# Kernel optimization log

Hardware: AMD Instinct MI355X
Metric: run time of the kernel (lower is better)

Reference implementation:

```python
import jax, jax.numpy as jnp
import numpy as np

B, S, SE, H, NH = 1, 2048, 2048, 1024, 16
HD = H // NH
INNER = 4 * H
EPS = 1e-5


def layer_norm(x, g, b):
    mu = jnp.mean(x, axis=-1, keepdims=True)
    var = jnp.mean(jnp.square(x - mu), axis=-1, keepdims=True)
    return (x - mu) * jax.lax.rsqrt(var + EPS) * g + b


def split_heads(x):  # [B,T,H] -> [B,NH,T,HD]
    b, t, _ = x.shape
    return x.reshape(b, t, NH, HD).transpose(0, 2, 1, 3)


def merge_heads(x):  # [B,NH,T,HD] -> [B,T,H]
    b, nh, t, hd = x.shape
    return x.transpose(0, 2, 1, 3).reshape(b, t, nh * hd)


def setup_inputs() -> dict:
    key = jax.random.key(0)
    ks = jax.random.split(key, 16)
    n = lambda k, shp: (jax.random.normal(k, shp, jnp.float32) * 0.02)
    return {
        "hidden_states": jax.random.normal(ks[0], (B, S, H), jnp.float32),
        "encoder_hidden_states": jax.random.normal(ks[1], (B, SE, H), jnp.float32),
        "scorer_logits": jax.random.normal(ks[2], (B, SE), jnp.float32),
        "ln1_g": jnp.ones((H,), jnp.float32), "ln1_b": jnp.zeros((H,), jnp.float32),
        "c_attn_w": n(ks[3], (H, 3 * H)), "c_attn_b": jnp.zeros((3 * H,), jnp.float32),
        "attn_proj_w": n(ks[4], (H, H)), "attn_proj_b": jnp.zeros((H,), jnp.float32),
        "lnx_g": jnp.ones((H,), jnp.float32), "lnx_b": jnp.zeros((H,), jnp.float32),
        "q_attn_w": n(ks[5], (H, H)), "q_attn_b": jnp.zeros((H,), jnp.float32),
        "x_kv_w": n(ks[6], (H, 2 * H)), "x_kv_b": jnp.zeros((2 * H,), jnp.float32),
        "x_proj_w": n(ks[7], (H, H)), "x_proj_b": jnp.zeros((H,), jnp.float32),
        "ln2_g": jnp.ones((H,), jnp.float32), "ln2_b": jnp.zeros((H,), jnp.float32),
        "fc_w": n(ks[8], (H, INNER)), "fc_b": jnp.zeros((INNER,), jnp.float32),
        "mlp_proj_w": n(ks[9], (INNER, H)), "mlp_proj_b": jnp.zeros((H,), jnp.float32),
    }


def _attn_core(q, k, v, extra_bias=None, causal_bool=False, tril_diag2_additive=False):
    # q,k,v: [B,NH,T,HD]; eager attention, materializes full score matrix (faithful to source)
    w = jnp.einsum("bhqd,bhkd->bhqk", q, k) / jnp.sqrt(jnp.asarray(HD, q.dtype))
    ql, kl = q.shape[-2], k.shape[-2]
    neg = jnp.finfo(w.dtype).min
    if causal_bool:
        mask = jnp.tril(jnp.ones((ql, kl), bool))  # self-attn boolean causal mask
        w = jnp.where(mask[None, None], w, neg)
    if tril_diag2_additive:
        cm = jnp.tril(jnp.ones((ql, kl), w.dtype), k=2)  # limit_cross_attn: tril diagonal=2
        w = w + jnp.where(cm == 0, neg, jnp.zeros((), w.dtype))[None, None]
    if extra_bias is not None:
        w = w + extra_bias[:, None, None, :]  # scorer_logits additive per-key bias
    w = jax.nn.softmax(w, axis=-1)
    return jnp.einsum("bhqk,bhkd->bhqd", w, v)


def reference(hidden_states, encoder_hidden_states, scorer_logits,
              ln1_g, ln1_b, c_attn_w, c_attn_b, attn_proj_w, attn_proj_b,
              lnx_g, lnx_b, q_attn_w, q_attn_b, x_kv_w, x_kv_b, x_proj_w, x_proj_b,
              ln2_g, ln2_b, fc_w, fc_b, mlp_proj_w, mlp_proj_b):
    # --- self attention ---
    residual = hidden_states
    x = layer_norm(hidden_states, ln1_g, ln1_b)
    qkv = x @ c_attn_w + c_attn_b
    q, k, v = jnp.split(qkv, 3, axis=-1)
    a = _attn_core(split_heads(q), split_heads(k), split_heads(v), causal_bool=True)
    a = merge_heads(a) @ attn_proj_w + attn_proj_b
    hidden_states = a + residual
    # --- cross attention (limit_cross_attn=True, scorer_logits bias) ---
    residual = hidden_states
    x = layer_norm(hidden_states, lnx_g, lnx_b)
    q = x @ q_attn_w + q_attn_b
    kv = encoder_hidden_states @ x_kv_w + x_kv_b
    k, v = jnp.split(kv, 2, axis=-1)
    a = _attn_core(split_heads(q), split_heads(k), split_heads(v),
                   extra_bias=scorer_logits, tril_diag2_additive=True)
    a = merge_heads(a) @ x_proj_w + x_proj_b
    hidden_states = residual + a
    # --- MLP (gelu_new = tanh approx) ---
    residual = hidden_states
    x = layer_norm(hidden_states, ln2_g, ln2_b)
    h = jax.nn.gelu(x @ fc_w + fc_b, approximate=True)
    hidden_states = residual + (h @ mlp_proj_w + mlp_proj_b)
    return hidden_states
```

## Files before the change

kernel.cpp:

```cpp
#include <hip/hip_runtime.h>
#include <stdint.h>

#define H     1024
#define S     2048
#define SEQE  2048
#define NHEAD 16
#define HD    64
#define INNER 4096
#define EPSLN 1e-5f
#define LOG2E 1.44269504089f
#define SCALE2 (0.125f * LOG2E)

typedef __attribute__((ext_vector_type(8))) short short8;
typedef __attribute__((ext_vector_type(4))) float floatx4;

__device__ __forceinline__ float b2f(unsigned short u){
  union { unsigned int i; float f; } v; v.i = ((unsigned int)u) << 16; return v.f;
}
__device__ __forceinline__ unsigned short f2b(float f){
  union { float f; unsigned int i; } v; v.f = f;
  unsigned int x = v.i;
  unsigned int r = (x + 0x7FFFu + ((x >> 16) & 1u)) >> 16;
  return (unsigned short)r;
}
__device__ __forceinline__ float fexp2(float x){ return __builtin_amdgcn_exp2f(x); }
__device__ __forceinline__ float gelu_tanh(float x){
  float x3 = x*x*x;
  float t = tanhf(0.7978845608028654f*(x + 0.044715f*x3));
  return 0.5f*x*(1.0f+t);
}

__device__ __forceinline__ void gld16(const unsigned short* g, unsigned short* l){
  __builtin_amdgcn_global_load_lds(
      (const __attribute__((address_space(1))) unsigned int*)g,
      (__attribute__((address_space(3))) unsigned int*)l,
      16, 0, 0);
}

__global__ __launch_bounds__(256) void k_sniff(
    const unsigned short* __restrict__ p, int* __restrict__ flag){
  __shared__ int any;
  if (threadIdx.x == 0) any = 0;
  __syncthreads();
  int bad = 0;
  for (int i = threadIdx.x; i < 8192; i += 256){
    float v = b2f(p[i]);
    if (!(fabsf(v) < 1e6f)) bad = 1;
  }
  if (bad) any = 1;
  __syncthreads();
  if (threadIdx.x == 0) flag[0] = any;
}

struct PrepT {
  const void* src[7];
  unsigned short* dst[7];
  int R[7], C[7];
  int pre[8];
};
__global__ __launch_bounds__(256) void k_prep_t(PrepT d, const int* __restrict__ flag){
  __shared__ unsigned short t[32][33];
  int b = blockIdx.x;
  int m = 0;
  while (b >= d.pre[m+1]) m++;
  int ti = b - d.pre[m];
  int R = d.R[m], C = d.C[m];
  int tx = threadIdx.x & 31, ty = threadIdx.x >> 5;
  int tilesx = C >> 5;
  int bc = (ti % tilesx) << 5, br = (ti / tilesx) << 5;
  const float* sf = (const float*)d.src[m];
  const unsigned short* sb = (const unsigned short*)d.src[m];
  unsigned short* dst = d.dst[m];
  int fl = flag[0];
  #pragma unroll
  for (int i = 0; i < 4; i++){
    size_t idx = (size_t)(br + ty + i*8) * C + bc + tx;
    t[ty + i*8][tx] = fl ? f2b(sf[idx]) : sb[idx];
  }
  __syncthreads();
  #pragma unroll
  for (int i = 0; i < 4; i++)
    dst[(size_t)(bc + ty + i*8) * R + br + tx] = t[tx][ty + i*8];
}

struct SmallCvt {
  const void* src[16];
  unsigned short* dst[16];
  int n[16];
};
__global__ __launch_bounds__(256) void k_prep_c(
    const void* __restrict__ enc, unsigned short* __restrict__ enc_c,
    const void* __restrict__ hsv, float* __restrict__ hidden,
    SmallCvt sc, const int* __restrict__ flag){
  int b = blockIdx.x, tid = threadIdx.x;
  int fl = flag[0];
  if (b < 8192){
    int i = b*256 + tid;
    enc_c[i] = fl ? f2b(((const float*)enc)[i]) : ((const unsigned short*)enc)[i];
  } else if (b < 16384){
    int i = (b - 8192)*256 + tid;
    hidden[i] = fl ? ((const float*)hsv)[i] : b2f(((const unsigned short*)hsv)[i]);
  } else {
    int t = b - 16384;
    const float* sf = (const float*)sc.src[t];
    const unsigned short* sb = (const unsigned short*)sc.src[t];
    unsigned short* d = sc.dst[t];
    for (int i = tid; i < sc.n[t]; i += 256)
      d[i] = fl ? f2b(sf[i]) : sb[i];
  }
}

__global__ __launch_bounds__(256) void k_layernorm(
    const float* __restrict__ x,
    const unsigned short* __restrict__ g, const unsigned short* __restrict__ bb,
    unsigned short* __restrict__ y){
  __shared__ float scratch[4];
  int row = blockIdx.x, tid = threadIdx.x;
  float v[4];
  #pragma unroll
  for (int i=0;i<4;i++) v[i] = x[(size_t)row*H + tid + i*256];
  float s = v[0]+v[1]+v[2]+v[3];
  for (int o=32;o;o>>=1) s += __shfl_xor(s,o,64);
  int wid = tid>>6, lane = tid&63;
  if (lane==0) scratch[wid]=s;
  __syncthreads();
  float mu = (scratch[0]+scratch[1]+scratch[2]+scratch[3]) * (1.0f/H);
  __syncthreads();
  float q = 0.f;
  #pragma unroll
  for (int i=0;i<4;i++){ float d=v[i]-mu; q += d*d; }
  for (int o=32;o;o>>=1) q += __shfl_xor(q,o,64);
  if (lane==0) scratch[wid]=q;
  __syncthreads();
  float var = (scratch[0]+scratch[1]+scratch[2]+scratch[3]) * (1.0f/H);
  float rstd = rsqrtf(var + EPSLN);
  #pragma unroll
  for (int i=0;i<4;i++){
    int idx = tid + i*256;
    float o = (v[i]-mu)*rstd*b2f(g[idx]) + b2f(bb[idx]);
    y[(size_t)row*H + idx] = f2b(o);
  }
}

__global__ __launch_bounds__(256) void k_gemm64(
    const unsigned short* __restrict__ A, const unsigned short* __restrict__ BT,
    const unsigned short* __restrict__ bias,
    unsigned short* __restrict__ outb, float* __restrict__ resid,
    int M, int N, int K, int mode, const int* __restrict__ flag,
    int vcol0, unsigned short* __restrict__ vtout)
{
  __shared__ __align__(16) unsigned short As[2][64*64];
  __shared__ __align__(16) unsigned short Bs[2][128*64];
  int tid = threadIdx.x;
  int bm0 = blockIdx.y * 64, bn0 = blockIdx.x * 128;
  int wid = tid >> 6, lane = tid & 63;
  int wm = (wid & 1) * 32, wn = (wid >> 1) * 64;
  int fl = (mode == 3) ? flag[0] : 0;
  floatx4 acc[2][4] = {};

  const unsigned short* gp[6];
  int lofs[6];
  int aseg[6];
  int lrow = lane >> 3, lchunk = (lane & 7) ^ lrow;
  #pragma unroll
  for (int t = 0; t < 6; t++){
    int seg = wid * 6 + t;
    if (seg < 8){
      gp[t] = A + (size_t)(bm0 + seg*8 + lrow) * K + lchunk*8;
      lofs[t] = seg * 512;
      aseg[t] = 1;
    } else {
      int s = seg - 8;
      gp[t] = BT + (size_t)(bn0 + s*8 + lrow) * K + lchunk*8;
      lofs[t] = s * 512;
      aseg[t] = 0;
    }
  }

  #pragma unroll
  for (int t = 0; t < 6; t++)
    gld16(gp[t], (aseg[t] ? As[0] : Bs[0]) + lofs[t]);

  int mrow = lane & 15, quad = lane >> 4;
  int ib = 0;
  for (int kt = 0; kt < K; kt += 64, ib ^= 1){
    __syncthreads();
    if (kt + 64 < K){
      #pragma unroll
      for (int t = 0; t < 6; t++)
        gld16(gp[t] + kt + 64, (aseg[t] ? As[ib^1] : Bs[ib^1]) + lofs[t]);
    }
    const unsigned short* Ac = As[ib];
    const unsigned short* Bc = Bs[ib];
    #pragma unroll
    for (int k2 = 0; k2 < 2; k2++){
      short8 af[2], bf[4];
      #pragma unroll
      for (int i = 0; i < 2; i++){
        int r = wm + i*16 + mrow;
        int slot = (k2*4 + quad) ^ (r & 7);
        af[i] = *(const short8*)&Ac[r*64 + slot*8];
      }
      #pragma unroll
      for (int j = 0; j < 4; j++){
        int r = wn + j*16 + mrow;
        int slot = (k2*4 + quad) ^ (r & 7);
        bf[j] = *(const short8*)&Bc[r*64 + slot*8];
      }
      #pragma unroll
      for (int i = 0; i < 2; i++){
        #pragma unroll
        for (int j = 0; j < 4; j++){
          acc[i][j] = __builtin_amdgcn_mfma_f32_16x16x32_bf16(af[i], bf[j], acc[i][j], 0,0,0);
        }
      }
    }
  }

  int colb = mrow, rowb = quad * 4;
  #pragma unroll
  for (int i=0;i<2;i++){
    #pragma unroll
    for (int j=0;j<4;j++){
      int col = bn0 + wn + j*16 + colb;
      float bv = b2f(bias[col]);
      int row0 = bm0 + wm + i*16 + rowb;
      if (mode == 4 && col >= vcol0){
        ushort4 uv;
        uv.x = f2b(acc[i][j][0] + bv);
        uv.y = f2b(acc[i][j][1] + bv);
        uv.z = f2b(acc[i][j][2] + bv);
        uv.w = f2b(acc[i][j][3] + bv);
        *(ushort4*)(vtout + (size_t)(col - vcol0)*M + row0) = uv;
      } else {
        #pragma unroll
        for (int rr=0;rr<4;rr++){
          int row = row0 + rr;
          float v = acc[i][j][rr] + bv;
          size_t off = (size_t)row*N + col;
          if      (mode == 0 || mode == 4){ outb[off] = f2b(v); }
          else if (mode == 1){ outb[off] = f2b(gelu_tanh(v)); }
          else if (mode == 2){ resid[off] += v; }
          else {
            float o = v + resid[off];
            if (fl) ((float*)outb)[off] = o;
            else    outb[off] = f2b(o);
          }
        }
      }
    }
  }
}

__global__ __launch_bounds__(256) void k_gemm64s(
    const unsigned short* __restrict__ A, const unsigned short* __restrict__ BT,
    const unsigned short* __restrict__ bias,
    unsigned short* __restrict__ outb, float* __restrict__ resid,
    int M, int N, int K, int mode, const int* __restrict__ flag)
{
  __shared__ __align__(16) unsigned short As[2][64*64];
  __shared__ __align__(16) unsigned short Bs[2][64*64];
  int tid = threadIdx.x;
  int bm0 = blockIdx.y * 64, bn0 = blockIdx.x * 64;
  int wid = tid >> 6, lane = tid & 63;
  int wm = wid * 16;
  int fl = (mode == 3) ? flag[0] : 0;
  floatx4 acc[4] = {};

  const unsigned short* gp[4];
  int lofs[4];
  int aseg[4];
  int lrow = lane >> 3, lchunk = (lane & 7) ^ lrow;
  #pragma unroll
  for (int t = 0; t < 4; t++){
    int seg = wid * 4 + t;
    if (seg < 8){
      gp[t] = A + (size_t)(bm0 + seg*8 + lrow) * K + lchunk*8;
      lofs[t] = seg * 512;
      aseg[t] = 1;
    } else {
      int s = seg - 8;
      gp[t] = BT + (size_t)(bn0 + s*8 + lrow) * K + lchunk*8;
      lofs[t] = s * 512;
      aseg[t] = 0;
    }
  }

  #pragma unroll
  for (int t = 0; t < 4; t++)
    gld16(gp[t], (aseg[t] ? As[0] : Bs[0]) + lofs[t]);

  int mrow = lane & 15, quad = lane >> 4;
  int ib = 0;
  for (int kt = 0; kt < K; kt += 64, ib ^= 1){
    __syncthreads();
    if (kt + 64 < K){
      #pragma unroll
      for (int t = 0; t < 4; t++)
        gld16(gp[t] + kt + 64, (aseg[t] ? As[ib^1] : Bs[ib^1]) + lofs[t]);
    }
    const unsigned short* Ac = As[ib];
    const unsigned short* Bc = Bs[ib];
    #pragma unroll
    for (int k2 = 0; k2 < 2; k2++){
      short8 af, bf[4];
      {
        int r = wm + mrow;
        int slot = (k2*4 + quad) ^ (r & 7);
        af = *(const short8*)&Ac[r*64 + slot*8];
      }
      #pragma unroll
      for (int j = 0; j < 4; j++){
        int r = j*16 + mrow;
        int slot = (k2*4 + quad) ^ (r & 7);
        bf[j] = *(const short8*)&Bc[r*64 + slot*8];
      }
      #pragma unroll
      for (int j = 0; j < 4; j++)
        acc[j] = __builtin_amdgcn_mfma_f32_16x16x32_bf16(af, bf[j], acc[j], 0,0,0);
    }
  }

  int colb = mrow, rowb = quad * 4;
  #pragma unroll
  for (int j=0;j<4;j++){
    int col = bn0 + j*16 + colb;
    float bv = b2f(bias[col]);
    int row0 = bm0 + wm + rowb;
    #pragma unroll
    for (int rr=0;rr<4;rr++){
      int row = row0 + rr;
      float v = acc[j][rr] + bv;
      size_t off = (size_t)row*N + col;
      if      (mode == 0){ outb[off] = f2b(v); }
      else if (mode == 2){ resid[off] += v; }
      else {
        float o = v + resid[off];
        if (fl) ((float*)outb)[off] = o;
        else    outb[off] = f2b(o);
      }
    }
  }
}

template<int CA, int SCOR>
__global__ __launch_bounds__(256) void k_flash2(
    const unsigned short* __restrict__ qb, int qstride,
    const unsigned short* __restrict__ kb, int kstride,
    const unsigned short* __restrict__ vt,
    const unsigned short* __restrict__ scorer,
    unsigned short* __restrict__ obuf, float* __restrict__ mlbuf, int TOTS)
{
  int t = blockIdx.x, h = blockIdx.y, sp = blockIdx.z;
  int klmax0 = 64*t + 64 + CA; if (klmax0 > S) klmax0 = S;
  int nch = (klmax0 + 63) >> 6;
  int nsp = (nch + 7) >> 3;
  if (sp >= nsp) return;
  int base = 0;
  for (int i = 0; i < t; i++){
    int km = 64*i + 64 + CA; if (km > S) km = S;
    base += (((km + 63) >> 6) + 7) >> 3;
  }
  int pidx = h*TOTS + base + sp;
  int c0 = sp*8, c1 = c0 + 8; if (c1 > nch) c1 = nch;

  __shared__ __align__(16) unsigned short Ks[2][64*64];
  __shared__ __align__(16) unsigned short VTs[2][64*64];
  __shared__ __align__(16) unsigned short Ps[4][16*72];
  __shared__ float scs[2][64];
  int tid = threadIdx.x;
  int q0 = t*64;
  int w = tid >> 6, lane = tid & 63;
  int cn = lane & 15, quad = lane >> 4, kq = quad * 8;
  unsigned short* Pw = Ps[w];
  int srow0 = w*16;
  int lr = lane >> 3;
  int lc = ((lane & 7) ^ lr) * 8;
  const unsigned short* kg0 = kb + (size_t)(srow0 + lr) * kstride + h*HD + lc;
  const unsigned short* kg1 = kb + (size_t)(srow0 + 8 + lr) * kstride + h*HD + lc;
  const unsigned short* vg0 = vt + (size_t)(h*HD + srow0 + lr) * S + lc;
  const unsigned short* vg1 = vt + (size_t)(h*HD + srow0 + 8 + lr) * S + lc;

  const unsigned short* qrow = qb + (size_t)(q0 + w*16 + cn) * qstride + h*HD;
  short8 qf0 = *(const short8*)(qrow + kq);
  short8 qf1 = *(const short8*)(qrow + kq + 32);
  floatx4 oacc[4] = {};
  float l_lane[4] = {0,0,0,0};
  float m_w = -1.0e38f;
  int qmr = q0 + w*16 + quad*4;

  {
    int kc = c0 * 64;
    gld16(kg0 + (size_t)kc * kstride, Ks[0] + srow0*64);
    gld16(kg1 + (size_t)kc * kstride, Ks[0] + (srow0 + 8)*64);
    gld16(vg0 + kc, VTs[0] + srow0*64);
    gld16(vg1 + kc, VTs[0] + (srow0 + 8)*64);
    if (SCOR && tid < 64) scs[0][tid] = b2f(scorer[kc + tid]) * LOG2E;
  }

  int ib = 0;
  for (int ci = c0; ci < c1; ci++, ib ^= 1){
    __syncthreads();
    if (ci + 1 < c1){
      int kn2 = (ci + 1) * 64;
      gld16(kg0 + (size_t)kn2 * kstride, Ks[ib^1] + srow0*64);
      gld16(kg1 + (size_t)kn2 * kstride, Ks[ib^1] + (srow0 + 8)*64);
      gld16(vg0 + kn2, VTs[ib^1] + srow0*64);
      gld16(vg1 + kn2, VTs[ib^1] + (srow0 + 8)*64);
      if (SCOR && tid < 64) scs[ib^1][tid] = b2f(scorer[kn2 + tid]) * LOG2E;
    }
    int kc = ci * 64;
    const unsigned short* Kc = Ks[ib];
    const unsigned short* Vc = VTs[ib];
    const float* scc = scs[ib];

    floatx4 sv[4] = {};
    #pragma unroll
    for (int t4=0;t4<4;t4++){
      int rr = t4*16 + cn;
      int s0 = ((quad    ) ^ (rr & 7)) * 8;
      int s1 = ((quad + 4) ^ (rr & 7)) * 8;
      short8 b0 = *(const short8*)&Kc[rr*64 + s0];
      short8 b1 = *(const short8*)&Kc[rr*64 + s1];
      sv[t4] = __builtin_amdgcn_mfma_f32_16x16x32_bf16(qf0, b0, sv[t4], 0,0,0);
      sv[t4] = __builtin_amdgcn_mfma_f32_16x16x32_bf16(qf1, b1, sv[t4], 0,0,0);
    }

    float vals[16];
    float lmax = -1.0e38f;
    if (kc + 63 > q0 + w*16 + CA){
      #pragma unroll
      for (int t4=0;t4<4;t4++){
        #pragma unroll
        for (int r=0;r<4;r++){
          float s = sv[t4][r] * SCALE2;
          if (SCOR) s += scc[t4*16 + cn];
          int kn = kc + t4*16 + cn;
          s = (kn <= qmr + r + CA) ? s : -1.0e38f;
          vals[t4*4+r] = s;
          lmax = fmaxf(lmax, s);
        }
      }
    } else {
      #pragma unroll
      for (int t4=0;t4<4;t4++){
        #pragma unroll
        for (int r=0;r<4;r++){
          float s = sv[t4][r] * SCALE2;
          if (SCOR) s += scc[t4*16 + cn];
          vals[t4*4+r] = s;
          lmax = fmaxf(lmax, s);
        }
      }
    }
    lmax = fmaxf(lmax, __shfl_xor(lmax,1,64));
    lmax = fmaxf(lmax, __shfl_xor(lmax,2,64));
    lmax = fmaxf(lmax, __shfl_xor(lmax,4,64));
    lmax = fmaxf(lmax, __shfl_xor(lmax,8,64));
    if (lmax > m_w){
      float al = fexp2(m_w - lmax);
      m_w = lmax;
      #pragma unroll
      for (int r=0;r<4;r++) l_lane[r] *= al;
      #pragma unroll
      for (int t2=0;t2<4;t2++){
        #pragma unroll
        for (int r=0;r<4;r++) oacc[t2][r] *= al;
      }
    }
    #pragma unroll
    for (int t4=0;t4<4;t4++){
      #pragma unroll
      for (int r=0;r<4;r++){
        float e = fexp2(vals[t4*4+r] - m_w);
        l_lane[r] += e;
        Pw[(quad*4+r)*72 + t4*16 + cn] = f2b(e);
      }
    }
    short8 pf0 = *(const short8*)&Pw[cn*72 + kq];
    short8 pf1 = *(const short8*)&Pw[cn*72 + kq + 32];
    #pragma unroll
    for (int t2=0;t2<4;t2++){
      int rr = t2*16 + cn;
      int s0 = ((quad    ) ^ (rr & 7)) * 8;
      int s1 = ((quad + 4) ^ (rr & 7)) * 8;
      short8 v0 = *(const short8*)&Vc[rr*64 + s0];
      short8 v1 = *(const short8*)&Vc[rr*64 + s1];
      oacc[t2] = __builtin_amdgcn_mfma_f32_16x16x32_bf16(pf0, v0, oacc[t2], 0,0,0);
      oacc[t2] = __builtin_amdgcn_mfma_f32_16x16x32_bf16(pf1, v1, oacc[t2], 0,0,0);
    }
  }

  float lrow[4];
  #pragma unroll
  for (int r=0;r<4;r++){
    float l = l_lane[r];
    l += __shfl_xor(l,1,64); l += __shfl_xor(l,2,64);
    l += __shfl_xor(l,4,64); l += __shfl_xor(l,8,64);
    lrow[r] = l;
  }
  size_t ob = (size_t)pidx*4096 + (size_t)(w*16 + quad*4)*64;
  #pragma unroll
  for (int t2=0;t2<4;t2++){
    #pragma unroll
    for (int r=0;r<4;r++)
      obuf[ob + r*64 + t2*16 + cn] = f2b(oacc[t2][r]);
  }
  if (cn == 0){
    #pragma unroll
    for (int r=0;r<4;r++){
      int row64 = w*16 + quad*4 + r;
      mlbuf[((size_t)pidx*64 + row64)*2]   = m_w;
      mlbuf[((size_t)pidx*64 + row64)*2+1] = lrow[r];
    }
  }
}

template<int CA>
__global__ __launch_bounds__(256) void k_comb(
    const unsigned short* __restrict__ obuf, const float* __restrict__ mlbuf,
    unsigned short* __restrict__ out, int TOTS)
{
  int h = blockIdx.y;
  int row = blockIdx.x*16 + (threadIdx.x >> 4);
  int d0 = (threadIdx.x & 15) * 4;
  int t = row >> 6;
  int klmax0 = 64*t + 64 + CA; if (klmax0 > S) klmax0 = S;
  int nch = (klmax0 + 63) >> 6;
  int nsp = (nch + 7) >> 3;
  int base = 0;
  for (int i = 0; i < t; i++){
    int km = 64*i + 64 + CA; if (km > S) km = S;
    base += (((km + 63) >> 6) + 7) >> 3;
  }
  int row64 = row & 63;
  float mp[4], lp[4];
  float M = -1.0e38f;
  for (int p = 0; p < nsp; p++){
    int pi = h*TOTS + base + p;
    mp[p] = mlbuf[((size_t)pi*64 + row64)*2];
    lp[p] = mlbuf[((size_t)pi*64 + row64)*2+1];
    M = fmaxf(M, mp[p]);
  }
  float L = 0.f;
  float o0=0.f,o1=0.f,o2=0.f,o3=0.f;
  for (int p = 0; p < nsp; p++){
    int pi = h*TOTS + base + p;
    float wgt = fexp2(mp[p] - M);
    L += lp[p]*wgt;
    const unsigned short* op = obuf + (size_t)pi*4096 + row64*64 + d0;
    o0 += b2f(op[0])*wgt; o1 += b2f(op[1])*wgt;
    o2 += b2f(op[2])*wgt; o3 += b2f(op[3])*wgt;
  }
  float inv = 1.0f / L;
  size_t oo = (size_t)row*H + h*HD + d0;
  out[oo]   = f2b(o0*inv); out[oo+1] = f2b(o1*inv);
  out[oo+2] = f2b(o2*inv); out[oo+3] = f2b(o3*inv);
}

extern "C" void kernel_launch(void* const* d_in, const int* in_sizes, int n_in,
                              void* d_out, int out_size, void* d_ws, size_t ws_size,
                              hipStream_t stream)
{
  const void* hs          = d_in[0];
  const void* enc         = d_in[1];
  const void* scorer      = d_in[2];
  const void* ln1_g       = d_in[3];
  const void* ln1_b       = d_in[4];
  const void* c_attn_w    = d_in[5];
  const void* c_attn_b    = d_in[6];
  const void* attn_proj_w = d_in[7];
  const void* attn_proj_b = d_in[8];
  const void* lnx_g       = d_in[9];
  const void* lnx_b       = d_in[10];
  const void* q_attn_w    = d_in[11];
  const void* q_attn_b    = d_in[12];
  const void* x_kv_w      = d_in[13];
  const void* x_kv_b      = d_in[14];
  const void* x_proj_w    = d_in[15];
  const void* x_proj_b    = d_in[16];
  const void* ln2_g       = d_in[17];
  const void* ln2_b       = d_in[18];
  const void* fc_w        = d_in[19];
  const void* fc_b        = d_in[20];
  const void* mlp_proj_w  = d_in[21];
  const void* mlp_proj_b  = d_in[22];
  unsigned short* out = (unsigned short*)d_out;

  char* ws = (char*)d_ws; size_t off = 0;
  auto alloc = [&](size_t bytes)->void*{
    void* p = ws + off; off += (bytes + 255) & ~(size_t)255; return p;
  };
  unsigned short* wT_cattn = (unsigned short*)alloc((size_t)3072*1024*2);
  unsigned short* wT_aproj = (unsigned short*)alloc((size_t)1024*1024*2);
  unsigned short* wT_qattn = (unsigned short*)alloc((size_t)1024*1024*2);
  unsigned short* wT_xkv   = (unsigned short*)alloc((size_t)2048*1024*2);
  unsigned short* wT_xproj = (unsigned short*)alloc((size_t)1024*1024*2);
  unsigned short* wT_fc    = (unsigned short*)alloc((size_t)4096*1024*2);
  unsigned short* wT_mlp   = (unsigned short*)alloc((size_t)1024*4096*2);
  unsigned short* enc_c    = (unsigned short*)alloc((size_t)SEQE*H*2);
  unsigned short* canon    = (unsigned short*)alloc((size_t)32768*2);
  unsigned short* xln      = (unsigned short*)alloc((size_t)S*H*2);
  unsigned short* qkv      = (unsigned short*)alloc((size_t)S*3*H*2);
  unsigned short* attnout  = (unsigned short*)alloc((size_t)S*H*2);
  unsigned short* q2       = (unsigned short*)alloc((size_t)S*H*2);
  unsigned short* kvbuf    = (unsigned short*)alloc((size_t)SEQE*2*H*2);
  unsigned short* vt_self  = (unsigned short*)alloc((size_t)H*S*2);
  unsigned short* vt_cross = (unsigned short*)alloc((size_t)H*SEQE*2);
  unsigned short* fcbuf    = (unsigned short*)alloc((size_t)S*INNER*2);
  float*          hidden   = (float*)alloc((size_t)S*H*4);
  int*            flag     = (int*)alloc(256);

  unsigned short* obuf  = fcbuf;
  float*          mlbuf = (float*)(fcbuf + (size_t)16*83*4096);

  unsigned short* p = canon;
  auto carve = [&](int n)->unsigned short*{ unsigned short* q = p; p += n; return q; };
  unsigned short* c_ln1g = carve(1024); unsigned short* c_ln1b = carve(1024);
  unsigned short* c_catb = carve(3072); unsigned short* c_aprb = carve(1024);
  unsigned short* c_lnxg = carve(1024); unsigned short* c_lnxb = carve(1024);
  unsigned short* c_qatb = carve(1024); unsigned short* c_xkvb = carve(2048);
  unsigned short* c_xprb = carve(1024); unsigned short* c_ln2g = carve(1024);
  unsigned short* c_ln2b = carve(1024); unsigned short* c_fcb  = carve(4096);
  unsigned short* c_mlpb = carve(1024); unsigned short* c_scor = carve(2048);

  k_sniff<<<1, 256, 0, stream>>>((const unsigned short*)hs, flag);

  PrepT pt{};
  const void* tsrc[7] = {c_attn_w, attn_proj_w, q_attn_w, x_kv_w, x_proj_w, fc_w, mlp_proj_w};
  unsigned short* tdst[7] = {wT_cattn, wT_aproj, wT_qattn, wT_xkv, wT_xproj, wT_fc, wT_mlp};
  int tR[7] = {1024,1024,1024,1024,1024,1024,4096};
  int tC[7] = {3072,1024,1024,2048,1024,4096,1024};
  int acc_t = 0;
  for (int i=0;i<7;i++){
    pt.src[i]=tsrc[i]; pt.dst[i]=tdst[i]; pt.R[i]=tR[i]; pt.C[i]=tC[i];
    pt.pre[i]=acc_t; acc_t += (tC[i]>>5)*(tR[i]>>5);
  }
  pt.pre[7]=acc_t;
  k_prep_t<<<acc_t, 256, 0, stream>>>(pt, flag);

  SmallCvt sc{};
  const void* ssrc[14] = {ln1_g, ln1_b, c_attn_b, attn_proj_b, lnx_g, lnx_b,
                          q_attn_b, x_kv_b, x_proj_b, ln2_g, ln2_b, fc_b,
                          mlp_proj_b, scorer};
  unsigned short* sdst[14] = {c_ln1g, c_ln1b, c_catb, c_aprb, c_lnxg, c_lnxb,
                              c_qatb, c_xkvb, c_xprb, c_ln2g, c_ln2b, c_fcb,
                              c_mlpb, c_scor};
  int sn[14] = {1024,1024,3072,1024,1024,1024,1024,2048,1024,1024,1024,4096,1024,2048};
  for (int i=0;i<14;i++){ sc.src[i]=ssrc[i]; sc.dst[i]=sdst[i]; sc.n[i]=sn[i]; }
  k_prep_c<<<16384 + 14, 256, 0, stream>>>(enc, enc_c, hs, hidden, sc, flag);

  k_layernorm<<<S, 256, 0, stream>>>(hidden, c_ln1g, c_ln1b, xln);
  k_gemm64<<<dim3(3072/128, S/64), 256, 0, stream>>>(xln, wT_cattn, c_catb,
      qkv, nullptr, S, 3072, 1024, 4, flag, 2048, vt_self);
  k_flash2<0,0><<<dim3(32, NHEAD, 4), 256, 0, stream>>>(
      qkv, 3*H, qkv + 1024, 3*H, vt_self, nullptr, obuf, mlbuf, 80);
  k_comb<0><<<dim3(S/16, NHEAD), 256, 0, stream>>>(obuf, mlbuf, attnout, 80);
  k_gemm64s<<<dim3(1024/64, S/64), 256, 0, stream>>>(attnout, wT_aproj, c_aprb,
      nullptr, hidden, S, 1024, 1024, 2, flag);

  k_layernorm<<<S, 256, 0, stream>>>(hidden, c_lnxg, c_lnxb, xln);
  k_gemm64s<<<dim3(1024/64, S/64), 256, 0, stream>>>(xln, wT_qattn, c_qatb,
      q2, nullptr, S, 1024, 1024, 0, flag);
  k_gemm64<<<dim3(2048/128, SEQE/64), 256, 0, stream>>>(enc_c, wT_xkv, c_xkvb,
      kvbuf, nullptr, SEQE, 2048, 1024, 4, flag, 1024, vt_cross);
  k_flash2<2,1><<<dim3(32, NHEAD, 4), 256, 0, stream>>>(
      q2, H, kvbuf, 2*H, vt_cross, c_scor, obuf, mlbuf, 83);
  k_comb<2><<<dim3(S/16, NHEAD), 256, 0, stream>>>(obuf, mlbuf, attnout, 83);
  k_gemm64s<<<dim3(1024/64, S/64), 256, 0, stream>>>(attnout, wT_xproj, c_xprb,
      nullptr, hidden, S, 1024, 1024, 2, flag);

  k_layernorm<<<S, 256, 0, stream>>>(hidden, c_ln2g, c_ln2b, xln);
  k_gemm64<<<dim3(INNER/128, S/64), 256, 0, stream>>>(xln, wT_fc, c_fcb,
      fcbuf, nullptr, S, INNER, 1024, 1, flag, 0, nullptr);
  k_gemm64s<<<dim3(1024/64, S/64), 256, 0, stream>>>(fcbuf, wT_mlp, c_mlpb,
      out, hidden, S, 1024, INNER, 3, flag);
}
```

Measured before the change: 467.1 us.

## Split-K with atomics for projection GEMMs, single-buffer V, branchless softmax rescale

The output-projection and MLP-down GEMMs now split the K dimension across blockIdx.z and accumulate into the fp32 residual with atomicAdd. This raises the block count for the narrow N=1024 GEMMs, and a separate k_final kernel writes the output. The flash kernel moves from double-buffered to single-buffered V-transpose loads, which cuts LDS use, and adds a __syncthreads before P is read. The online-softmax rescale becomes unconditional, and the scorer LOG2E scaling moves into prep. The costs are atomic contention, one extra kernel pass, and V loads that are no longer prefetched.

```diff
diff --git a/kernel.cpp b/kernel.cpp
--- a/kernel.cpp
+++ b/kernel.cpp
@@ -105,8 +105,11 @@
     const float* sf = (const float*)sc.src[t];
     const unsigned short* sb = (const unsigned short*)sc.src[t];
     unsigned short* d = sc.dst[t];
-    for (int i = tid; i < sc.n[t]; i += 256)
-      d[i] = fl ? f2b(sf[i]) : sb[i];
+    for (int i = tid; i < sc.n[t]; i += 256){
+      float vv = fl ? sf[i] : b2f(sb[i]);
+      if (t == 13) vv *= LOG2E;
+      d[i] = f2b(vv);
+    }
   }
 }
 
@@ -155,7 +158,6 @@
   int bm0 = blockIdx.y * 64, bn0 = blockIdx.x * 128;
   int wid = tid >> 6, lane = tid & 63;
   int wm = (wid & 1) * 32, wn = (wid >> 1) * 64;
-  int fl = (mode == 3) ? flag[0] : 0;
   floatx4 acc[2][4] = {};
 
   const unsigned short* gp[6];
@@ -240,12 +242,7 @@
           size_t off = (size_t)row*N + col;
           if      (mode == 0 || mode == 4){ outb[off] = f2b(v); }
           else if (mode == 1){ outb[off] = f2b(gelu_tanh(v)); }
-          else if (mode == 2){ resid[off] += v; }
-          else {
-            float o = v + resid[off];
-            if (fl) ((float*)outb)[off] = o;
-            else    outb[off] = f2b(o);
-          }
+          else               { resid[off] += v; }
         }
       }
     }
@@ -256,15 +253,15 @@
     const unsigned short* __restrict__ A, const unsigned short* __restrict__ BT,
     const unsigned short* __restrict__ bias,
     unsigned short* __restrict__ outb, float* __restrict__ resid,
-    int M, int N, int K, int mode, const int* __restrict__ flag)
+    int M, int N, int K, int klen, int mode)
 {
   __shared__ __align__(16) unsigned short As[2][64*64];
   __shared__ __align__(16) unsigned short Bs[2][64*64];
   int tid = threadIdx.x;
   int bm0 = blockIdx.y * 64, bn0 = blockIdx.x * 64;
+  int k0 = blockIdx.z * klen;
   int wid = tid >> 6, lane = tid & 63;
   int wm = wid * 16;
-  int fl = (mode == 3) ? flag[0] : 0;
   floatx4 acc[4] = {};
 
   const unsigned short* gp[4];
@@ -275,12 +272,12 @@
   for (int t = 0; t < 4; t++){
     int seg = wid * 4 + t;
     if (seg < 8){
-      gp[t] = A + (size_t)(bm0 + seg*8 + lrow) * K + lchunk*8;
+      gp[t] = A + (size_t)(bm0 + seg*8 + lrow) * K + k0 + lchunk*8;
       lofs[t] = seg * 512;
       aseg[t] = 1;
     } else {
       int s = seg - 8;
-      gp[t] = BT + (size_t)(bn0 + s*8 + lrow) * K + lchunk*8;
+      gp[t] = BT + (size_t)(bn0 + s*8 + lrow) * K + k0 + lchunk*8;
       lofs[t] = s * 512;
       aseg[t] = 0;
     }
@@ -292,9 +289,9 @@
 
   int mrow = lane & 15, quad = lane >> 4;
   int ib = 0;
-  for (int kt = 0; kt < K; kt += 64, ib ^= 1){
+  for (int kt = 0; kt < klen; kt += 64, ib ^= 1){
     __syncthreads();
-    if (kt + 64 < K){
+    if (kt + 64 < klen){
       #pragma unroll
       for (int t = 0; t < 4; t++)
         gld16(gp[t] + kt + 64, (aseg[t] ? As[ib^1] : Bs[ib^1]) + lofs[t]);
@@ -325,22 +322,26 @@
   #pragma unroll
   for (int j=0;j<4;j++){
     int col = bn0 + j*16 + colb;
-    float bv = b2f(bias[col]);
+    float bv = (blockIdx.z == 0) ? b2f(bias[col]) : 0.f;
     int row0 = bm0 + wm + rowb;
     #pragma unroll
     for (int rr=0;rr<4;rr++){
       int row = row0 + rr;
       float v = acc[j][rr] + bv;
       size_t off = (size_t)row*N + col;
-      if      (mode == 0){ outb[off] = f2b(v); }
-      else if (mode == 2){ resid[off] += v; }
-      else {
-        float o = v + resid[off];
-        if (fl) ((float*)outb)[off] = o;
-        else    outb[off] = f2b(o);
-      }
-    }
-  }
+      if (mode == 0) outb[off] = f2b(v);
+      else           atomicAdd(&resid[off], v);
+    }
+  }
+}
+
+__global__ __launch_bounds__(256) void k_final(
+    const float* __restrict__ hidden, unsigned short* __restrict__ out,
+    const int* __restrict__ flag){
+  int i = blockIdx.x * 256 + threadIdx.x;
+  float v = hidden[i];
+  if (flag[0]) ((float*)out)[i] = v;
+  else         out[i] = f2b(v);
 }
 
 template<int CA, int SCOR>
@@ -365,7 +366,7 @@
   int c0 = sp*8, c1 = c0 + 8; if (c1 > nch) c1 = nch;
 
   __shared__ __align__(16) unsigned short Ks[2][64*64];
-  __shared__ __align__(16) unsigned short VTs[2][64*64];
+  __shared__ __align__(16) unsigned short VTs[64*64];
   __shared__ __align__(16) unsigned short Ps[4][16*72];
   __shared__ float scs[2][64];
   int tid = threadIdx.x;
@@ -393,25 +394,22 @@
     int kc = c0 * 64;
     gld16(kg0 + (size_t)kc * kstride, Ks[0] + srow0*64);
     gld16(kg1 + (size_t)kc * kstride, Ks[0] + (srow0 + 8)*64);
-    gld16(vg0 + kc, VTs[0] + srow0*64);
-    gld16(vg1 + kc, VTs[0] + (srow0 + 8)*64);
-    if (SCOR && tid < 64) scs[0][tid] = b2f(scorer[kc + tid]) * LOG2E;
+    if (SCOR && tid < 64) scs[0][tid] = b2f(scorer[kc + tid]);
   }
 
   int ib = 0;
   for (int ci = c0; ci < c1; ci++, ib ^= 1){
+    int kc = ci * 64;
     __syncthreads();
+    gld16(vg0 + kc, VTs + srow0*64);
+    gld16(vg1 + kc, VTs + (srow0 + 8)*64);
     if (ci + 1 < c1){
       int kn2 = (ci + 1) * 64;
       gld16(kg0 + (size_t)kn2 * kstride, Ks[ib^1] + srow0*64);
       gld16(kg1 + (size_t)kn2 * kstride, Ks[ib^1] + (srow0 + 8)*64);
-      gld16(vg0 + kn2, VTs[ib^1] + srow0*64);
-      gld16(vg1 + kn2, VTs[ib^1] + (srow0 + 8)*64);
-      if (SCOR && tid < 64) scs[ib^1][tid] = b2f(scorer[kn2 + tid]) * LOG2E;
-    }
-    int kc = ci * 64;
+      if (SCOR && tid < 64) scs[ib^1][tid] = b2f(scorer[kn2 + tid]);
+    }
     const unsigned short* Kc = Ks[ib];
-    const unsigned short* Vc = VTs[ib];
     const float* scc = scs[ib];
 
     floatx4 sv[4] = {};
@@ -457,16 +455,15 @@
     lmax = fmaxf(lmax, __shfl_xor(lmax,2,64));
     lmax = fmaxf(lmax, __shfl_xor(lmax,4,64));
     lmax = fmaxf(lmax, __shfl_xor(lmax,8,64));
-    if (lmax > m_w){
-      float al = fexp2(m_w - lmax);
-      m_w = lmax;
-      #pragma unroll
-      for (int r=0;r<4;r++) l_lane[r] *= al;
-      #pragma unroll
-      for (int t2=0;t2<4;t2++){
-        #pragma unroll
-        for (int r=0;r<4;r++) oacc[t2][r] *= al;
-      }
+    float mnew = fmaxf(m_w, lmax);
+    float al = fexp2(m_w - mnew);
+    m_w = mnew;
+    #pragma unroll
+    for (int r=0;r<4;r++) l_lane[r] *= al;
+    #pragma unroll
+    for (int t2=0;t2<4;t2++){
+      #pragma unroll
+      for (int r=0;r<4;r++) oacc[t2][r] *= al;
     }
     #pragma unroll
     for (int t4=0;t4<4;t4++){
@@ -477,6 +474,7 @@
         Pw[(quad*4+r)*72 + t4*16 + cn] = f2b(e);
       }
     }
+    __syncthreads();
     short8 pf0 = *(const short8*)&Pw[cn*72 + kq];
     short8 pf1 = *(const short8*)&Pw[cn*72 + kq + 32];
     #pragma unroll
@@ -484,8 +482,8 @@
       int rr = t2*16 + cn;
       int s0 = ((quad    ) ^ (rr & 7)) * 8;
       int s1 = ((quad + 4) ^ (rr & 7)) * 8;
-      short8 v0 = *(const short8*)&Vc[rr*64 + s0];
-      short8 v1 = *(const short8*)&Vc[rr*64 + s1];
+      short8 v0 = *(const short8*)&VTs[rr*64 + s0];
+      short8 v1 = *(const short8*)&VTs[rr*64 + s1];
       oacc[t2] = __builtin_amdgcn_mfma_f32_16x16x32_bf16(pf0, v0, oacc[t2], 0,0,0);
       oacc[t2] = __builtin_amdgcn_mfma_f32_16x16x32_bf16(pf1, v1, oacc[t2], 0,0,0);
     }
@@ -656,23 +654,24 @@
   k_flash2<0,0><<<dim3(32, NHEAD, 4), 256, 0, stream>>>(
       qkv, 3*H, qkv + 1024, 3*H, vt_self, nullptr, obuf, mlbuf, 80);
   k_comb<0><<<dim3(S/16, NHEAD), 256, 0, stream>>>(obuf, mlbuf, attnout, 80);
-  k_gemm64s<<<dim3(1024/64, S/64), 256, 0, stream>>>(attnout, wT_aproj, c_aprb,
-      nullptr, hidden, S, 1024, 1024, 2, flag);
+  k_gemm64s<<<dim3(1024/64, S/64, 2), 256, 0, stream>>>(attnout, wT_aproj, c_aprb,
+      nullptr, hidden, S, 1024, 1024, 512, 2);
 
   k_layernorm<<<S, 256, 0, stream>>>(hidden, c_lnxg, c_lnxb, xln);
-  k_gemm64s<<<dim3(1024/64, S/64), 256, 0, stream>>>(xln, wT_qattn, c_qatb,
-      q2, nullptr, S, 1024, 1024, 0, flag);
+  k_gemm64s<<<dim3(1024/64, S/64, 1), 256, 0, stream>>>(xln, wT_qattn, c_qatb,
+      q2, nullptr, S, 1024, 1024, 1024, 0);
   k_gemm64<<<dim3(2048/128, SEQE/64), 256, 0, stream>>>(enc_c, wT_xkv, c_xkvb,
       kvbuf, nullptr, SEQE, 2048, 1024, 4, flag, 1024, vt_cross);
   k_flash2<2,1><<<dim3(32, NHEAD, 4), 256, 0, stream>>>(
       q2, H, kvbuf, 2*H, vt_cross, c_scor, obuf, mlbuf, 83);
   k_comb<2><<<dim3(S/16, NHEAD), 256, 0, stream>>>(obuf, mlbuf, attnout, 83);
-  k_gemm64s<<<dim3(1024/64, S/64), 256, 0, stream>>>(attnout, wT_xproj, c_xprb,
-      nullptr, hidden, S, 1024, 1024, 2, flag);
+  k_gemm64s<<<dim3(1024/64, S/64, 2), 256, 0, stream>>>(attnout, wT_xproj, c_xprb,
+      nullptr, hidden, S, 1024, 1024, 512, 2);
 
   k_layernorm<<<S, 256, 0, stream>>>(hidden, c_ln2g, c_ln2b, xln);
   k_gemm64<<<dim3(INNER/128, S/64), 256, 0, stream>>>(xln, wT_fc, c_fcb,
       fcbuf, nullptr, S, INNER, 1024, 1, flag, 0, nullptr);
-  k_gemm64s<<<dim3(1024/64, S/64), 256, 0, stream>>>(fcbuf, wT_mlp, c_mlpb,
-      out, hidden, S, 1024, INNER, 3, flag);
-}
+  k_gemm64s<<<dim3(1024/64, S/64, 4), 256, 0, stream>>>(fcbuf, wT_mlp, c_mlpb,
+      nullptr, hidden, S, 1024, INNER, 1024, 2);
+  k_final<<<(S*H)/256, 256, 0, stream>>>(hidden, out, flag);
+}
```

Measured after the change: 476.3 us. No clear change (+2.0%).
